# Kernel optimization log

Measured on AMD Instinct MI355X. Metric: run time of the kernel, lower is better.

The kernel has to match this reference:

```python
import jax, jax.numpy as jnp
import numpy as np


def setup_inputs() -> dict:
    key = jax.random.key(0)
    k1, k2 = jax.random.split(key)
    x = jax.random.normal(k1, (32, 128, 64, 64), dtype=jnp.float32)
    # weights: [out_channels, in_channels, k, k], as in nn.Parameter(torch.randn(...))
    weights = jax.random.normal(k2, (256, 128, 3, 3), dtype=jnp.float32)
    return {"x": x, "weights": weights}


def reference(x, weights):
    # output[b,o,i,j] = sum_{c,kh,kw} x[b,c,i+kh,j+kw] * weights[o,c,kh,kw]
    # == standard VALID cross-correlation (weights shared across locations).
    return jax.lax.conv_general_dilated(
        x, weights,
        window_strides=(1, 1),
        padding="VALID",
        dimension_numbers=("NCHW", "OIHW", "NCHW"),
    )
```

## Files before the change

kernel.cpp:

```cpp
#include <hip/hip_runtime.h>
#include <hip/hip_bf16.h>

typedef __bf16 bf16_t;
typedef __bf16 bf16x8 __attribute__((ext_vector_type(8)));
typedef float f32x16 __attribute__((ext_vector_type(16)));
typedef float f32x4v __attribute__((ext_vector_type(4)));

#define NB 32
#define CIN 128
#define HIN 64
#define WIN 64
#define OCH 256
#define OHW 62

__global__ __launch_bounds__(256) void conv_wt_kernel(const float* __restrict__ w,
                                                      bf16_t* __restrict__ wt2) {
  int t = blockIdx.x * 256 + threadIdx.x;
  int lane = t & 63;
  int kk = (t >> 6) & 7;
  int o5 = (t >> 9) & 7;
  int tap = t >> 12;
  int o = o5 * 32 + (lane & 31);
  int c0 = kk * 16 + (lane >> 5) * 8;
  const float* src = w + (size_t)o * 1152 + (size_t)c0 * 9 + tap;
  bf16x8 v;
#pragma unroll
  for (int e = 0; e < 8; ++e) v[e] = (bf16_t)src[e * 9];
  *(bf16x8*)(wt2 + (size_t)t * 8) = v;
}

__global__ __launch_bounds__(256, 2) void conv_main_kernel(const float* __restrict__ x,
                                                           const bf16_t* __restrict__ wt2,
                                                           float* __restrict__ out) {
  __shared__ __align__(16) char xs[256 * 256];

  const int tid = threadIdx.x;
  const int lane = tid & 63;
  const int l31 = lane & 31;
  const int lhi = lane >> 5;
  const int wid = tid >> 6;
  const int b = blockIdx.y;
  const int i0 = blockIdx.x * 2;

  const char* wt2b = (const char*)wt2;

  f32x16 acc[2][4];
#pragma unroll
  for (int m = 0; m < 2; ++m)
#pragma unroll
    for (int n = 0; n < 4; ++n)
#pragma unroll
      for (int r = 0; r < 16; ++r) acc[m][n][r] = 0.f;

  {
    const int c8 = tid & 7;
    const int wq = (tid >> 3) & 15;
    const int rr = tid >> 7;
#pragma unroll
    for (int hp = 0; hp < 2; ++hp) {
#pragma unroll
      for (int cp = 0; cp < 2; ++cp) {
        const int h_loc = hp * 2 + rr;
        const float* src = x + (((size_t)b * CIN + cp * 64 + c8 * 8) * HIN +
                                (i0 + h_loc)) * WIN + wq * 4;
        f32x4v xr[8];
#pragma unroll
        for (int dc = 0; dc < 8; ++dc)
          xr[dc] = *(const f32x4v*)(src + (size_t)dc * (HIN * WIN));
#pragma unroll
        for (int dw = 0; dw < 4; ++dw) {
          bf16x8 v;
#pragma unroll
          for (int dc = 0; dc < 8; ++dc) v[dc] = (bf16_t)xr[dc][dw];
          int row = h_loc * 64 + wq * 4 + dw;
          *(bf16x8*)(xs + row * 256 +
                     ((cp * 128 + c8 * 16) ^ ((row & 15) << 4))) = v;
        }
      }
    }
  }
  __syncthreads();

#define LOAD_AH(dst, s, half)                                                  \
  {                                                                            \
    _Pragma("unroll") for (int m = 0; m < 2; ++m)                              \
        _Pragma("unroll") for (int kk4 = 0; kk4 < 4; ++kk4)                    \
            dst[m * 4 + kk4] = *(const bf16x8*)(                               \
                wt2b + ((((size_t)(s) * 8 + wid * 2 + m) * 8 + (half) * 4 +    \
                         kk4) * 64 + lane) * 16);                              \
  }

#define COMP(A, s, half)                                                       \
  {                                                                            \
    const int kh_ = (s) / 3, kw_ = (s) % 3;                                    \
    _Pragma("unroll") for (int kk4 = 0; kk4 < 4; ++kk4) {                      \
      bf16x8 bb[4];                                                            \
      _Pragma("unroll") for (int n = 0; n < 4; ++n) {                          \
        int row = ((n >> 1) + kh_) * 64 + (n & 1) * 32 + l31 + kw_;            \
        row = row < 256 ? row : 255;      \
        bb[n] = *(const bf16x8*)(                                              \
            xs + row * 256 +                                                   \
            ((((half) * 4 + kk4) * 32 + lhi * 16) ^ ((row & 15) << 4)));       \
      }                                                                        \
      __builtin_amdgcn_s_setprio(1);                                           \
      _Pragma("unroll") for (int n = 0; n < 4; ++n)                            \
          _Pragma("unroll") for (int m = 0; m < 2; ++m)                        \
              acc[m][n] = __builtin_amdgcn_mfma_f32_32x32x16_bf16(             \
                  A[m * 4 + kk4], bb[n], acc[m][n], 0, 0, 0);                  \
      __builtin_amdgcn_s_setprio(0);                                           \
    }                                                                          \
  }

  bf16x8 A0[8], A1[8];
  LOAD_AH(A0, 0, 0);
#pragma unroll
  for (int t = 0; t < 9; ++t) {
    LOAD_AH(A1, t, 1);
    COMP(A0, t, 0);
    if (t < 8) LOAD_AH(A0, t + 1, 0);
    COMP(A1, t, 1);
  }

#pragma unroll
  for (int n = 0; n < 4; ++n) {
    int j = (n & 1) * 32 + l31;
    int i = i0 + (n >> 1);
    if (j < 62) {
#pragma unroll
      for (int m = 0; m < 2; ++m) {
#pragma unroll
        for (int r = 0; r < 16; ++r) {
          int o = (wid * 2 + m) * 32 + (r & 3) + 8 * (r >> 2) + 4 * lhi;
          out[((size_t)(b * 256 + o) * OHW + i) * OHW + j] = acc[m][n][r];
        }
      }
    }
  }
#undef LOAD_AH
#undef COMP
}

extern "C" void kernel_launch(void* const* d_in, const int* in_sizes, int n_in,
                              void* d_out, int out_size, void* d_ws, size_t ws_size,
                              hipStream_t stream) {
  const float* x = (const float*)d_in[0];
  const float* w = (const float*)d_in[1];
  float* out = (float*)d_out;

  bf16_t* wt2 = (bf16_t*)d_ws;

  conv_wt_kernel<<<dim3(144), dim3(256), 0, stream>>>(w, wt2);
  conv_main_kernel<<<dim3(31, NB), dim3(256), 0, stream>>>(x, wt2, out);
}
```

Before: 258.3 us.

## Compute one output row per block to cut LDS and raise occupancy

Each block now produces a single output row instead of two. It stages 3 input rows (48 KB LDS instead of 64 KB), halves the accumulators, and declares 3 blocks per CU. The grid doubles to 62x32, and the A/B fragment loads are pipelined in 36 finer steps. The cost is that every block still loads the full weight set per tap, so weight reads per output double, and 3 input rows are read to produce 1 output row, where before 4 rows produced 2.

```diff
diff --git a/kernel.cpp b/kernel.cpp
--- a/kernel.cpp
+++ b/kernel.cpp
@@ -29,10 +29,10 @@
   *(bf16x8*)(wt2 + (size_t)t * 8) = v;
 }
 
-__global__ __launch_bounds__(256, 2) void conv_main_kernel(const float* __restrict__ x,
+__global__ __launch_bounds__(256, 3) void conv_main_kernel(const float* __restrict__ x,
                                                            const bf16_t* __restrict__ wt2,
                                                            float* __restrict__ out) {
-  __shared__ __align__(16) char xs[256 * 256];
+  __shared__ __align__(16) char xs[192 * 256];
 
   const int tid = threadIdx.x;
   const int lane = tid & 63;
@@ -40,104 +40,107 @@
   const int lhi = lane >> 5;
   const int wid = tid >> 6;
   const int b = blockIdx.y;
-  const int i0 = blockIdx.x * 2;
+  const int i0 = blockIdx.x;
 
   const char* wt2b = (const char*)wt2;
 
-  f32x16 acc[2][4];
+  f32x16 acc[2][2];
 #pragma unroll
   for (int m = 0; m < 2; ++m)
 #pragma unroll
-    for (int n = 0; n < 4; ++n)
+    for (int n = 0; n < 2; ++n)
 #pragma unroll
       for (int r = 0; r < 16; ++r) acc[m][n][r] = 0.f;
 
   {
-    const int c8 = tid & 7;
-    const int wq = (tid >> 3) & 15;
-    const int rr = tid >> 7;
+    const int c8 = tid & 15;
+    const int wq = tid >> 4;
 #pragma unroll
-    for (int hp = 0; hp < 2; ++hp) {
+    for (int h = 0; h < 3; ++h) {
+      const float* src = x + (((size_t)b * CIN + c8 * 8) * HIN + (i0 + h)) * WIN + wq * 4;
+      f32x4v xr[8];
 #pragma unroll
-      for (int cp = 0; cp < 2; ++cp) {
-        const int h_loc = hp * 2 + rr;
-        const float* src = x + (((size_t)b * CIN + cp * 64 + c8 * 8) * HIN +
-                                (i0 + h_loc)) * WIN + wq * 4;
-        f32x4v xr[8];
+      for (int dc = 0; dc < 8; ++dc)
+        xr[dc] = *(const f32x4v*)(src + (size_t)dc * (HIN * WIN));
 #pragma unroll
-        for (int dc = 0; dc < 8; ++dc)
-          xr[dc] = *(const f32x4v*)(src + (size_t)dc * (HIN * WIN));
+      for (int dw = 0; dw < 4; ++dw) {
+        bf16x8 v;
 #pragma unroll
-        for (int dw = 0; dw < 4; ++dw) {
-          bf16x8 v;
-#pragma unroll
-          for (int dc = 0; dc < 8; ++dc) v[dc] = (bf16_t)xr[dc][dw];
-          int row = h_loc * 64 + wq * 4 + dw;
-          *(bf16x8*)(xs + row * 256 +
-                     ((cp * 128 + c8 * 16) ^ ((row & 15) << 4))) = v;
-        }
+        for (int dc = 0; dc < 8; ++dc) v[dc] = (bf16_t)xr[dc][dw];
+        int row = h * 64 + wq * 4 + dw;
+        *(bf16x8*)(xs + row * 256 + ((c8 * 16) ^ ((row & 15) << 4))) = v;
       }
     }
   }
   __syncthreads();
 
-#define LOAD_AH(dst, s, half)                                                  \
+#define LOAD_A2(dst, s)                                                        \
   {                                                                            \
+    const int tap_ = (s) >> 2, kkp_ = (s) & 3;                                 \
     _Pragma("unroll") for (int m = 0; m < 2; ++m)                              \
-        _Pragma("unroll") for (int kk4 = 0; kk4 < 4; ++kk4)                    \
-            dst[m * 4 + kk4] = *(const bf16x8*)(                               \
-                wt2b + ((((size_t)(s) * 8 + wid * 2 + m) * 8 + (half) * 4 +    \
-                         kk4) * 64 + lane) * 16);                              \
+        _Pragma("unroll") for (int k2 = 0; k2 < 2; ++k2)                       \
+            dst[m * 2 + k2] = *(const bf16x8*)(                                \
+                wt2b + ((((size_t)tap_ * 8 + wid * 2 + m) * 8 + kkp_ * 2 +     \
+                         k2) * 64 + lane) * 16);                               \
   }
 
-#define COMP(A, s, half)                                                       \
+#define LOAD_B2(dst, s)                                                        \
   {                                                                            \
-    const int kh_ = (s) / 3, kw_ = (s) % 3;                                    \
-    _Pragma("unroll") for (int kk4 = 0; kk4 < 4; ++kk4) {                      \
-      bf16x8 bb[4];                                                            \
-      _Pragma("unroll") for (int n = 0; n < 4; ++n) {                          \
-        int row = ((n >> 1) + kh_) * 64 + (n & 1) * 32 + l31 + kw_;            \
-        row = row < 256 ? row : 255;      \
-        bb[n] = *(const bf16x8*)(                                              \
-            xs + row * 256 +                                                   \
-            ((((half) * 4 + kk4) * 32 + lhi * 16) ^ ((row & 15) << 4)));       \
-      }                                                                        \
-      __builtin_amdgcn_s_setprio(1);                                           \
-      _Pragma("unroll") for (int n = 0; n < 4; ++n)                            \
-          _Pragma("unroll") for (int m = 0; m < 2; ++m)                        \
-              acc[m][n] = __builtin_amdgcn_mfma_f32_32x32x16_bf16(             \
-                  A[m * 4 + kk4], bb[n], acc[m][n], 0, 0, 0);                  \
-      __builtin_amdgcn_s_setprio(0);                                           \
+    const int tap_ = (s) >> 2, kkp_ = (s) & 3;                                 \
+    const int kh_ = tap_ / 3, kw_ = tap_ % 3;                                  \
+    _Pragma("unroll") for (int n = 0; n < 2; ++n) {                            \
+      int row = kh_ * 64 + n * 32 + l31 + kw_;                                 \
+      row = row < 192 ? row : 191;        \
+      _Pragma("unroll") for (int k2 = 0; k2 < 2; ++k2)                         \
+          dst[n * 2 + k2] = *(const bf16x8*)(                                  \
+              xs + row * 256 +                                                 \
+              ((((kkp_ * 2 + k2) * 32) + lhi * 16) ^ ((row & 15) << 4)));      \
     }                                                                          \
   }
 
-  bf16x8 A0[8], A1[8];
-  LOAD_AH(A0, 0, 0);
+#define COMP8(A, B)                                                            \
+  {                                                                            \
+    __builtin_amdgcn_s_setprio(1);                                             \
+    _Pragma("unroll") for (int k2 = 0; k2 < 2; ++k2)                           \
+        _Pragma("unroll") for (int n = 0; n < 2; ++n)                          \
+            _Pragma("unroll") for (int m = 0; m < 2; ++m)                      \
+                acc[m][n] = __builtin_amdgcn_mfma_f32_32x32x16_bf16(           \
+                    A[m * 2 + k2], B[n * 2 + k2], acc[m][n], 0, 0, 0);         \
+    __builtin_amdgcn_s_setprio(0);                                             \
+  }
+
+  bf16x8 Aa[4], Ab[4], Ba[4], Bb[4];
+  LOAD_A2(Aa, 0);
+  LOAD_B2(Ba, 0);
 #pragma unroll
-  for (int t = 0; t < 9; ++t) {
-    LOAD_AH(A1, t, 1);
-    COMP(A0, t, 0);
-    if (t < 8) LOAD_AH(A0, t + 1, 0);
-    COMP(A1, t, 1);
+  for (int s = 0; s < 36; s += 2) {
+    LOAD_A2(Ab, s + 1);
+    LOAD_B2(Bb, s + 1);
+    COMP8(Aa, Ba);
+    if (s + 2 < 36) {
+      LOAD_A2(Aa, s + 2);
+      LOAD_B2(Ba, s + 2);
+    }
+    COMP8(Ab, Bb);
   }
 
 #pragma unroll
-  for (int n = 0; n < 4; ++n) {
-    int j = (n & 1) * 32 + l31;
-    int i = i0 + (n >> 1);
+  for (int n = 0; n < 2; ++n) {
+    int j = n * 32 + l31;
     if (j < 62) {
 #pragma unroll
       for (int m = 0; m < 2; ++m) {
 #pragma unroll
         for (int r = 0; r < 16; ++r) {
           int o = (wid * 2 + m) * 32 + (r & 3) + 8 * (r >> 2) + 4 * lhi;
-          out[((size_t)(b * 256 + o) * OHW + i) * OHW + j] = acc[m][n][r];
+          out[((size_t)(b * 256 + o) * OHW + i0) * OHW + j] = acc[m][n][r];
         }
       }
     }
   }
-#undef LOAD_AH
-#undef COMP
+#undef LOAD_A2
+#undef LOAD_B2
+#undef COMP8
 }
 
 extern "C" void kernel_launch(void* const* d_in, const int* in_sizes, int n_in,
@@ -150,5 +153,5 @@
   bf16_t* wt2 = (bf16_t*)d_ws;
 
   conv_wt_kernel<<<dim3(144), dim3(256), 0, stream>>>(w, wt2);
-  conv_main_kernel<<<dim3(31, NB), dim3(256), 0, stream>>>(x, wt2, out);
+  conv_main_kernel<<<dim3(62, NB), dim3(256), 0, stream>>>(x, wt2, out);
 }
```

After: 243.5 us. 5.7% less time.
